# Kernel optimization log

Measured on AMD Instinct MI355X. Metric: run time of the kernel, lower is better.

## Reference

```python
import jax, jax.numpy as jnp
import numpy as np

N = 192    # num_nodes == number of trees
M = 256    # max_node_number (feature width per tree level)
D = 1024   # tree depth (NATree.shape[1])
K = M - N + 1  # Conv2 kernel size


def setup_inputs() -> dict:
    key = jax.random.key(0)
    k1, k2, k3, k4, k5, k6 = jax.random.split(key, 6)
    s = 0.05
    NATree = jax.random.normal(k1, (N, D, M), jnp.float32)
    W = jax.random.normal(k2, (M, M, 2), jnp.float32) * s   # Conv1d weight [out, in, kernel=2]
    b = jax.random.normal(k3, (M,), jnp.float32) * s        # Conv1d bias
    x = jax.random.normal(k4, (N, M), jnp.float32) * s      # self.x parameter
    W2 = jax.random.normal(k5, (K,), jnp.float32) * s       # Conv2 weight (out=1,in=1,kernel=K)
    b2 = jax.random.normal(k6, (), jnp.float32) * s         # Conv2 bias
    return {"NATree": NATree, "W": W, "b": b, "x": x, "W2": W2, "b2": b2}


def reference(NATree, W, b, x, W2, b2):
    # Conv1d(k=2) on cat([row_j, h]) splits into two MxM matmuls:
    #   h_new = W0 @ row_j + W1 @ h + b + sigmoid(row_j)
    W0 = W[:, :, 0]  # multiplies row_j (first position in concat)
    W1 = W[:, :, 1]  # multiplies carried state h
    rows = NATree[:, :-1, :]  # [N, D-1, M], levels j = 0 .. D-2
    # Precompute the per-level additive term in one batched matmul.
    u = jnp.einsum('ndm,km->ndk', rows, W0) + b + jax.nn.sigmoid(rows)  # [N, D-1, M]
    h0 = NATree[:, -1, :]  # [N, M], initial state = last tree level
    # Walk levels j = D-2 down to 0.
    u_seq = jnp.flip(u, axis=1).transpose(1, 0, 2)  # [D-1, N, M]

    def step(h, u_j):
        return u_j + h @ W1.T, None

    h_fin, _ = jax.lax.scan(step, h0, u_seq)  # [N, M]
    res = jax.nn.relu(h_fin + x)  # [N, M]
    # Conv2: 1-ch cross-correlation, kernel K, output length M-K+1 = N.
    out = jax.lax.conv_general_dilated(
        res[:, None, :], W2[None, None, :], window_strides=(1,), padding='VALID') + b2
    return jax.nn.sigmoid(out[:, 0, :])  # [N, N]
```

## Files before the change

kernel.cpp:

```cpp
#include <hip/hip_runtime.h>
#include <hip/hip_bf16.h>
#include <cstddef>

#define DN 192
#define DM 256
#define DD 1024
#define DK 65
#define OUTW 192

using f32x4 = __attribute__((ext_vector_type(4))) float;
using s16x8 = __attribute__((ext_vector_type(8))) short;

__device__ __forceinline__ float sigm(float v) { return 1.0f / (1.0f + __expf(-v)); }
__device__ __forceinline__ unsigned short f2b(float f) {
    __hip_bfloat16 h = __float2bfloat16(f);
    return *reinterpret_cast<unsigned short*>(&h);
}
__device__ __forceinline__ float b2f(unsigned short s) {
    __hip_bfloat16 h = *reinterpret_cast<__hip_bfloat16*>(&s);
    return __bfloat162float(h);
}

#define OFF_QF   0u
#define OFF_A2   65536u
#define OFF_A4   131072u
#define OFF_A8   196608u
#define OFF_A16  262144u
#define OFF_A32  327680u
#define OFF_A64  393216u
#define OFF_QB   458752u
#define OFF_W0B  491520u
#define OFF_P8B  524288u
#define OFF_P64B 557056u
#define OFF_SA1  589824u
#define OFF_SA2  3735552u
#define MFMA_NEED_BYTES 18087936ULL

__global__ __launch_bounds__(256) void k_prep2(const float* __restrict__ W,
                                               float* __restrict__ ws) {
    const int bid = blockIdx.x, t = threadIdx.x;
    if (bid < 256) {
        const int c = bid, m = t;
        ws[OFF_QF + m * 256 + c] = W[(size_t)(c * 256 + m) * 2 + 1];
    } else {
        const int which = (bid - 256) >> 5;
        const int e = ((bid - 256) & 31) * 256 + t;
        const int ct = e >> 9, ks = (e >> 6) & 7, l = e & 63;
        const int c = ct * 16 + (l & 15);
        const int mb = ks * 32 + (l >> 4) * 8;
        s16x8 pk;
#pragma unroll
        for (int j = 0; j < 8; ++j)
            pk[j] = (short)f2b(W[(size_t)(c * 256 + mb + j) * 2 + (which ? 0 : 1)]);
        float* dst = ws + (which ? OFF_W0B : OFF_QB);
        reinterpret_cast<s16x8*>(dst)[e] = pk;
    }
}

__global__ __launch_bounds__(256) void k_sq256(const float* __restrict__ A,
                                               float* __restrict__ C,
                                               ushort* __restrict__ bfrag) {
    __shared__ float ar[256];
    const int r0 = blockIdx.x, k = threadIdx.x;
    ar[k] = A[r0 * 256 + k];
    __syncthreads();
    float a0 = 0.f, a1 = 0.f, a2 = 0.f, a3 = 0.f;
    for (int m = 0; m < 256; m += 8) {
        a0 += ar[m + 0] * A[(m + 0) * 256 + k] + ar[m + 4] * A[(m + 4) * 256 + k];
        a1 += ar[m + 1] * A[(m + 1) * 256 + k] + ar[m + 5] * A[(m + 5) * 256 + k];
        a2 += ar[m + 2] * A[(m + 2) * 256 + k] + ar[m + 6] * A[(m + 6) * 256 + k];
        a3 += ar[m + 3] * A[(m + 3) * 256 + k] + ar[m + 7] * A[(m + 7) * 256 + k];
    }
    const float v = (a0 + a1) + (a2 + a3);
    C[r0 * 256 + k] = v;
    if (bfrag) {
        const int entry = ((k >> 4) * 8 + (r0 >> 5)) * 64 + ((r0 >> 3) & 3) * 16 + (k & 15);
        bfrag[entry * 8 + (r0 & 7)] = f2b(v);
    }
}

__global__ __launch_bounds__(512, 4) void k_fused(const float* __restrict__ NAT,
                                                  const float* __restrict__ bvec,
                                                  const float* __restrict__ ws,
                                                  ushort* __restrict__ SA1) {
    __shared__ short Rl[2][8][66][8];
    __shared__ short Sl[2][2][8][64][8];
    const int rt2 = blockIdx.x;
    const int grp = blockIdx.y;
    const int tid = threadIdx.x;
    const int w = tid >> 6, l = tid & 63;
    const int n0 = rt2 * 32;
    const ushort* W0b = reinterpret_cast<const ushort*>(ws + OFF_W0B);
    const ushort* Qb  = reinterpret_cast<const ushort*>(ws + OFF_QB);

    s16x8 qreg[2][8];
#pragma unroll
    for (int c = 0; c < 2; ++c)
#pragma unroll
        for (int ks = 0; ks < 8; ++ks)
            qreg[c][ks] = *reinterpret_cast<const s16x8*>(Qb + (((2 * w + c) * 8 + ks) * 64 + l) * 8);

    const int srow = tid >> 4;
    const int sks  = (tid >> 1) & 7;
    const int shalf = tid & 1;
    const float* sbase = NAT + (size_t)(n0 + srow) * DD * DM + sks * 32 + shalf * 16;

    float4 rv0, rv1, rv2, rv3;
    {
        const float* p = sbase + (size_t)(grp * 8 + 7) * DM;
        rv0 = *reinterpret_cast<const float4*>(p + 0);
        rv1 = *reinterpret_cast<const float4*>(p + 4);
        rv2 = *reinterpret_cast<const float4*>(p + 8);
        rv3 = *reinterpret_cast<const float4*>(p + 12);
    }
    const float bcol0 = bvec[w * 32 + (l & 15)];
    const float bcol1 = bvec[w * 32 + 16 + (l & 15)];

    f32x4 acc[2][2];
    int cur = 0;
    for (int it = 0; it < 8; ++it) {
        const int d = grp * 8 + 7 - it;
        {
            const int g0 = shalf * 2;
            s16x8 pk0, pk1;
            pk0[0] = (short)f2b(rv0.x); pk0[1] = (short)f2b(rv0.y);
            pk0[2] = (short)f2b(rv0.z); pk0[3] = (short)f2b(rv0.w);
            pk0[4] = (short)f2b(rv1.x); pk0[5] = (short)f2b(rv1.y);
            pk0[6] = (short)f2b(rv1.z); pk0[7] = (short)f2b(rv1.w);
            pk1[0] = (short)f2b(rv2.x); pk1[1] = (short)f2b(rv2.y);
            pk1[2] = (short)f2b(rv2.z); pk1[3] = (short)f2b(rv2.w);
            pk1[4] = (short)f2b(rv3.x); pk1[5] = (short)f2b(rv3.y);
            pk1[6] = (short)f2b(rv3.z); pk1[7] = (short)f2b(rv3.w);
            *reinterpret_cast<s16x8*>(&Rl[srow >> 4][sks][(srow & 15) + 16 * g0][0]) = pk0;
            *reinterpret_cast<s16x8*>(&Rl[srow >> 4][sks][(srow & 15) + 16 * (g0 + 1)][0]) = pk1;
        }
        if (it < 7) {
            const float* p = sbase + (size_t)(d - 1) * DM;
            rv0 = *reinterpret_cast<const float4*>(p + 0);
            rv1 = *reinterpret_cast<const float4*>(p + 4);
            rv2 = *reinterpret_cast<const float4*>(p + 8);
            rv3 = *reinterpret_cast<const float4*>(p + 12);
        }
        __syncthreads();

        if (grp == 127 && it == 0) {
#pragma unroll
            for (int rt = 0; rt < 2; ++rt)
#pragma unroll
                for (int c = 0; c < 2; ++c) {
                    const int col = w * 32 + c * 16 + (l & 15);
#pragma unroll
                    for (int r = 0; r < 4; ++r) {
                        const int n = n0 + rt * 16 + (l >> 4) * 4 + r;
                        acc[rt][c][r] = NAT[((size_t)n * DD + (DD - 1)) * DM + col];
                    }
                }
        } else {
#pragma unroll
            for (int rt = 0; rt < 2; ++rt)
#pragma unroll
                for (int c = 0; c < 2; ++c) {
                    const int col = w * 32 + c * 16 + (l & 15);
                    const int ksm = col >> 5, sl = 16 * ((col >> 3) & 3), jb = col & 7;
                    const float bc = c ? bcol1 : bcol0;
#pragma unroll
                    for (int r = 0; r < 4; ++r) {
                        const int row15 = (l >> 4) * 4 + r;
                        const unsigned short sv = (unsigned short)Rl[rt][ksm][row15 + sl][jb];
                        acc[rt][c][r] = bc + sigm(b2f(sv));
                    }
                }
#pragma unroll
            for (int ks = 0; ks < 8; ++ks) {
                const s16x8 gb0 = *reinterpret_cast<const s16x8*>(W0b + (((2 * w + 0) * 8 + ks) * 64 + l) * 8);
                const s16x8 gb1 = *reinterpret_cast<const s16x8*>(W0b + (((2 * w + 1) * 8 + ks) * 64 + l) * 8);
                const s16x8 a0 = *reinterpret_cast<const s16x8*>(&Rl[0][ks][l][0]);
                const s16x8 a1 = *reinterpret_cast<const s16x8*>(&Rl[1][ks][l][0]);
                acc[0][0] = __builtin_amdgcn_mfma_f32_16x16x32_bf16(a0, gb0, acc[0][0], 0, 0, 0);
                acc[0][1] = __builtin_amdgcn_mfma_f32_16x16x32_bf16(a0, gb1, acc[0][1], 0, 0, 0);
                acc[1][0] = __builtin_amdgcn_mfma_f32_16x16x32_bf16(a1, gb0, acc[1][0], 0, 0, 0);
                acc[1][1] = __builtin_amdgcn_mfma_f32_16x16x32_bf16(a1, gb1, acc[1][1], 0, 0, 0);
            }
        }
        if (it > 0) {
#pragma unroll
            for (int ks = 0; ks < 8; ++ks) {
                const s16x8 s0 = *reinterpret_cast<const s16x8*>(&Sl[cur][0][ks][l][0]);
                const s16x8 s1 = *reinterpret_cast<const s16x8*>(&Sl[cur][1][ks][l][0]);
                acc[0][0] = __builtin_amdgcn_mfma_f32_16x16x32_bf16(s0, qreg[0][ks], acc[0][0], 0, 0, 0);
                acc[0][1] = __builtin_amdgcn_mfma_f32_16x16x32_bf16(s0, qreg[1][ks], acc[0][1], 0, 0, 0);
                acc[1][0] = __builtin_amdgcn_mfma_f32_16x16x32_bf16(s1, qreg[0][ks], acc[1][0], 0, 0, 0);
                acc[1][1] = __builtin_amdgcn_mfma_f32_16x16x32_bf16(s1, qreg[1][ks], acc[1][1], 0, 0, 0);
            }
        }
        if (it < 7) {
#pragma unroll
            for (int rt = 0; rt < 2; ++rt)
#pragma unroll
                for (int c = 0; c < 2; ++c) {
                    const int col = w * 32 + c * 16 + (l & 15);
                    const int sl = 16 * ((col >> 3) & 3), jb = col & 7;
#pragma unroll
                    for (int r = 0; r < 4; ++r) {
                        const int row15 = (l >> 4) * 4 + r;
                        Sl[cur ^ 1][rt][w][row15 + sl][jb] = (short)f2b(acc[rt][c][r]);
                    }
                }
            __syncthreads();
            cur ^= 1;
        }
    }

#pragma unroll
    for (int rt = 0; rt < 2; ++rt)
#pragma unroll
        for (int c = 0; c < 2; ++c) {
            const size_t base = (((size_t)grp * 12 + (rt2 * 2 + rt)) * 16 + (2 * w + c)) * 64 + l;
            ushort4 o;
            o.x = f2b(acc[rt][c][0]); o.y = f2b(acc[rt][c][1]);
            o.z = f2b(acc[rt][c][2]); o.w = f2b(acc[rt][c][3]);
            reinterpret_cast<ushort4*>(SA1)[base] = o;
        }
}

__global__ __launch_bounds__(512) void k_scan(const void* __restrict__ Vin, int in_bf16,
                                              const float* __restrict__ ws, unsigned qb_off,
                                              int nsteps,
                                              void* __restrict__ OutC, int out_bf16,
                                              const float* __restrict__ xin,
                                              const float* __restrict__ W2,
                                              const float* __restrict__ b2p,
                                              float* __restrict__ outF) {
    __shared__ __align__(16) char smem[33856];
    short (*Sl)[2][8][64][8] = reinterpret_cast<short (*)[2][8][64][8]>(smem);
    float (*resl)[260]       = reinterpret_cast<float (*)[260]>(smem);
    float* w2l               = reinterpret_cast<float*>(smem + 33280);
    const int rt2 = blockIdx.x;
    const int grp = blockIdx.y;
    const int tid = threadIdx.x;
    const int w = tid >> 6, l = tid & 63;
    const ushort* Qb = reinterpret_cast<const ushort*>(ws + qb_off);

    s16x8 qreg[2][8];
#pragma unroll
    for (int c = 0; c < 2; ++c)
#pragma unroll
        for (int ks = 0; ks < 8; ++ks)
            qreg[c][ks] = *reinterpret_cast<const s16x8*>(Qb + (((2 * w + c) * 8 + ks) * 64 + l) * 8);

    f32x4 acc[2][2];
    int cur = 0;
    for (int it = 0; it < nsteps; ++it) {
        const int d = grp * nsteps + (nsteps - 1) - it;
#pragma unroll
        for (int rt = 0; rt < 2; ++rt)
#pragma unroll
            for (int c = 0; c < 2; ++c) {
                const size_t base = (((size_t)d * 12 + (rt2 * 2 + rt)) * 16 + (2 * w + c)) * 64 + l;
                if (in_bf16) {
                    const ushort4 v = reinterpret_cast<const ushort4*>(Vin)[base];
                    acc[rt][c][0] = b2f(v.x); acc[rt][c][1] = b2f(v.y);
                    acc[rt][c][2] = b2f(v.z); acc[rt][c][3] = b2f(v.w);
                } else {
                    acc[rt][c] = reinterpret_cast<const f32x4*>(Vin)[base];
                }
            }
        if (it > 0) {
#pragma unroll
            for (int ks = 0; ks < 8; ++ks) {
                const s16x8 a0 = *reinterpret_cast<const s16x8*>(&Sl[cur][0][ks][l][0]);
                const s16x8 a1 = *reinterpret_cast<const s16x8*>(&Sl[cur][1][ks][l][0]);
                acc[0][0] = __builtin_amdgcn_mfma_f32_16x16x32_bf16(a0, qreg[0][ks], acc[0][0], 0, 0, 0);
                acc[0][1] = __builtin_amdgcn_mfma_f32_16x16x32_bf16(a0, qreg[1][ks], acc[0][1], 0, 0, 0);
                acc[1][0] = __builtin_amdgcn_mfma_f32_16x16x32_bf16(a1, qreg[0][ks], acc[1][0], 0, 0, 0);
                acc[1][1] = __builtin_amdgcn_mfma_f32_16x16x32_bf16(a1, qreg[1][ks], acc[1][1], 0, 0, 0);
            }
        }
        if (it < nsteps - 1) {
#pragma unroll
            for (int rt = 0; rt < 2; ++rt)
#pragma unroll
                for (int c = 0; c < 2; ++c) {
                    const int col = w * 32 + c * 16 + (l & 15);
                    const int sl = 16 * ((col >> 3) & 3), jb = col & 7;
#pragma unroll
                    for (int r = 0; r < 4; ++r) {
                        const int row15 = (l >> 4) * 4 + r;
                        Sl[cur ^ 1][rt][w][row15 + sl][jb] = (short)f2b(acc[rt][c][r]);
                    }
                }
            __syncthreads();
            cur ^= 1;
        }
    }

    if (outF == nullptr) {
#pragma unroll
        for (int rt = 0; rt < 2; ++rt)
#pragma unroll
            for (int c = 0; c < 2; ++c) {
                const size_t base = (((size_t)grp * 12 + (rt2 * 2 + rt)) * 16 + (2 * w + c)) * 64 + l;
                if (out_bf16) {
                    ushort4 o;
                    o.x = f2b(acc[rt][c][0]); o.y = f2b(acc[rt][c][1]);
                    o.z = f2b(acc[rt][c][2]); o.w = f2b(acc[rt][c][3]);
                    reinterpret_cast<ushort4*>(OutC)[base] = o;
                } else {
                    reinterpret_cast<f32x4*>(OutC)[base] = acc[rt][c];
                }
            }
    } else {
        if (tid < DK) w2l[tid] = W2[tid];
        __syncthreads();
#pragma unroll
        for (int rt = 0; rt < 2; ++rt)
#pragma unroll
            for (int c = 0; c < 2; ++c) {
                const int col = w * 32 + c * 16 + (l & 15);
#pragma unroll
                for (int r = 0; r < 4; ++r) {
                    const int row = rt * 16 + (l >> 4) * 4 + r;
                    const int n = rt2 * 32 + row;
                    const float v = acc[rt][c][r] + xin[(size_t)n * DM + col];
                    resl[row][col] = v > 0.f ? v : 0.f;
                }
            }
        __syncthreads();
        const float b2v = *b2p;
        const int k = tid & 255;
        for (int rr = tid >> 8; rr < 32; rr += 2) {
            if (k < OUTW) {
                float o = b2v;
#pragma unroll
                for (int i = 0; i < DK; ++i) o += resl[rr][k + i] * w2l[i];
                outF[(size_t)(rt2 * 32 + rr) * OUTW + k] = sigm(o);
            }
        }
    }
}

#define OCB 16
#define ONB 64
#define OR1 24
#define ORB1 8
#define OPSTR 260
#define O_W0T 0u
#define O_W1T 65536u
#define O_PW  131072u
#define O_S   (131072u + 5u*65536u)

__global__ __launch_bounds__(256) void k_prep_o(const float* __restrict__ W, float* __restrict__ ws) {
    const int m = blockIdx.x, k = threadIdx.x;
    const float2 w = *reinterpret_cast<const float2*>(W + (size_t)k * 512 + m * 2);
    ws[O_W0T + m * 256 + k] = w.x;
    ws[O_W1T + m * 256 + k] = w.y;
}

__global__ __launch_bounds__(256) void k_sq_o(const float* __restrict__ A, float* __restrict__ C) {
    __shared__ float ar[4][OPSTR];
    const int r0 = blockIdx.x * 4, k = threadIdx.x;
    for (int r = 0; r < 4; ++r) ar[r][k] = A[(r0 + r) * 256 + k];
    __syncthreads();
    float a0 = 0.f, a1 = 0.f, a2 = 0.f, a3 = 0.f;
    for (int m = 0; m < 256; m += 4) {
        const float p0 = A[(m + 0) * 256 + k], p1 = A[(m + 1) * 256 + k];
        const float p2 = A[(m + 2) * 256 + k], p3 = A[(m + 3) * 256 + k];
        float4 t;
        t = *reinterpret_cast<const float4*>(&ar[0][m]); a0 += t.x * p0 + t.y * p1 + t.z * p2 + t.w * p3;
        t = *reinterpret_cast<const float4*>(&ar[1][m]); a1 += t.x * p0 + t.y * p1 + t.z * p2 + t.w * p3;
        t = *reinterpret_cast<const float4*>(&ar[2][m]); a2 += t.x * p0 + t.y * p1 + t.z * p2 + t.w * p3;
        t = *reinterpret_cast<const float4*>(&ar[3][m]); a3 += t.x * p0 + t.y * p1 + t.z * p2 + t.w * p3;
    }
    C[(r0 + 0) * 256 + k] = a0; C[(r0 + 1) * 256 + k] = a1;
    C[(r0 + 2) * 256 + k] = a2; C[(r0 + 3) * 256 + k] = a3;
}

__global__ __launch_bounds__(256) void k_phase1_o(const float* __restrict__ NAT,
                                                  const float* __restrict__ bvec,
                                                  const float* __restrict__ ws,
                                                  float* __restrict__ Sall) {
    __shared__ float Sl[OR1 * OPSTR];
    __shared__ float Rl[OR1 * OPSTR];
    const int rb = blockIdx.x, bb = blockIdx.y, tid = threadIdx.x;
    const int tj = tid & 63, ti = tid >> 6, n0 = rb * OR1;
    const float* __restrict__ W0t = ws + O_W0T;
    const float* __restrict__ W1t = ws + O_W1T;
    const float4 bv = *reinterpret_cast<const float4*>(bvec + 4 * tj);
    float acc[6][4];
    for (int it = 0; it < OCB; ++it) {
        const int d = bb * OCB + (OCB - 1) - it;
#pragma unroll
        for (int q = 0; q < 6; ++q) {
            const int row = q * 4 + ti;
            const float4 v = *reinterpret_cast<const float4*>(NAT + ((size_t)(n0 + row) * DD + d) * DM + 4 * tj);
            *reinterpret_cast<float4*>(&Rl[row * OPSTR + 4 * tj]) = v;
        }
        __syncthreads();
        if (d == DD - 1) {
#pragma unroll
            for (int r = 0; r < 6; ++r) {
                const float4 v = *reinterpret_cast<const float4*>(&Rl[(ti * 6 + r) * OPSTR + 4 * tj]);
                acc[r][0] = v.x; acc[r][1] = v.y; acc[r][2] = v.z; acc[r][3] = v.w;
            }
        } else {
#pragma unroll
            for (int r = 0; r < 6; ++r) {
                const float4 v = *reinterpret_cast<const float4*>(&Rl[(ti * 6 + r) * OPSTR + 4 * tj]);
                acc[r][0] = bv.x + sigm(v.x); acc[r][1] = bv.y + sigm(v.y);
                acc[r][2] = bv.z + sigm(v.z); acc[r][3] = bv.w + sigm(v.w);
            }
            if (it == 0) {
#pragma unroll 2
                for (int m = 0; m < DM; m += 2) {
                    const float4 w0a = *reinterpret_cast<const float4*>(W0t + m * DM + 4 * tj);
                    const float4 w0b = *reinterpret_cast<const float4*>(W0t + (m + 1) * DM + 4 * tj);
#pragma unroll
                    for (int r = 0; r < 6; ++r) {
                        const float2 rv = *reinterpret_cast<const float2*>(&Rl[(ti * 6 + r) * OPSTR + m]);
                        acc[r][0] += rv.x * w0a.x + rv.y * w0b.x;
                        acc[r][1] += rv.x * w0a.y + rv.y * w0b.y;
                        acc[r][2] += rv.x * w0a.z + rv.y * w0b.z;
                        acc[r][3] += rv.x * w0a.w + rv.y * w0b.w;
                    }
                }
            } else {
#pragma unroll 2
                for (int m = 0; m < DM; m += 2) {
                    const float4 w0a = *reinterpret_cast<const float4*>(W0t + m * DM + 4 * tj);
                    const float4 w0b = *reinterpret_cast<const float4*>(W0t + (m + 1) * DM + 4 * tj);
                    const float4 w1a = *reinterpret_cast<const float4*>(W1t + m * DM + 4 * tj);
                    const float4 w1b = *reinterpret_cast<const float4*>(W1t + (m + 1) * DM + 4 * tj);
#pragma unroll
                    for (int r = 0; r < 6; ++r) {
                        const float2 rv = *reinterpret_cast<const float2*>(&Rl[(ti * 6 + r) * OPSTR + m]);
                        const float2 sv = *reinterpret_cast<const float2*>(&Sl[(ti * 6 + r) * OPSTR + m]);
                        acc[r][0] += rv.x * w0a.x + rv.y * w0b.x + sv.x * w1a.x + sv.y * w1b.x;
                        acc[r][1] += rv.x * w0a.y + rv.y * w0b.y + sv.x * w1a.y + sv.y * w1b.y;
                        acc[r][2] += rv.x * w0a.z + rv.y * w0b.z + sv.x * w1a.z + sv.y * w1b.z;
                        acc[r][3] += rv.x * w0a.w + rv.y * w0b.w + sv.x * w1a.w + sv.y * w1b.w;
                    }
                }
            }
        }
        __syncthreads();
#pragma unroll
        for (int r = 0; r < 6; ++r) {
            float4 v; v.x = acc[r][0]; v.y = acc[r][1]; v.z = acc[r][2]; v.w = acc[r][3];
            *reinterpret_cast<float4*>(&Sl[(ti * 6 + r) * OPSTR + 4 * tj]) = v;
        }
        __syncthreads();
    }
    float* dst = Sall + ((size_t)bb * DN + n0) * DM;
#pragma unroll
    for (int r = 0; r < 6; ++r) {
        float4 v; v.x = acc[r][0]; v.y = acc[r][1]; v.z = acc[r][2]; v.w = acc[r][3];
        *reinterpret_cast<float4*>(dst + (size_t)(ti * 6 + r) * DM + 4 * tj) = v;
    }
}

__global__ __launch_bounds__(256) void k_phase2_o(const float* __restrict__ Sall,
                                                  const float* __restrict__ P,
                                                  const float* __restrict__ x,
                                                  const float* __restrict__ W2,
                                                  const float* __restrict__ b2p,
                                                  float* __restrict__ out) {
    __shared__ float Tl[2][DM];
    __shared__ float resl[DM];
    const int n = blockIdx.x, k = threadIdx.x;
    float a = Sall[((size_t)(ONB - 1) * DN + n) * DM + k];
    Tl[0][k] = a;
    __syncthreads();
    int cur = 0;
    for (int b = ONB - 2; b >= 0; --b) {
        const float s0 = Sall[((size_t)b * DN + n) * DM + k];
        float a0 = 0.f, a1 = 0.f, a2 = 0.f, a3 = 0.f;
        for (int m = 0; m < DM; m += 8) {
            const float4 t0 = *reinterpret_cast<const float4*>(&Tl[cur][m]);
            const float4 t1 = *reinterpret_cast<const float4*>(&Tl[cur][m + 4]);
            a0 += t0.x * P[(m + 0) * DM + k] + t1.x * P[(m + 4) * DM + k];
            a1 += t0.y * P[(m + 1) * DM + k] + t1.y * P[(m + 5) * DM + k];
            a2 += t0.z * P[(m + 2) * DM + k] + t1.z * P[(m + 6) * DM + k];
            a3 += t0.w * P[(m + 3) * DM + k] + t1.w * P[(m + 7) * DM + k];
        }
        a = s0 + ((a0 + a1) + (a2 + a3));
        Tl[cur ^ 1][k] = a;
        __syncthreads();
        cur ^= 1;
    }
    const float b2v = *b2p;
    float r = a + x[(size_t)n * DM + k];
    resl[k] = r > 0.f ? r : 0.f;
    __syncthreads();
    if (k < OUTW) {
        float o = b2v;
#pragma unroll 5
        for (int i = 0; i < DK; ++i) o += resl[k + i] * W2[i];
        out[(size_t)n * OUTW + k] = sigm(o);
    }
}

extern "C" void kernel_launch(void* const* d_in, const int* in_sizes, int n_in,
                              void* d_out, int out_size, void* d_ws, size_t ws_size,
                              hipStream_t stream) {
    const float* NAT = (const float*)d_in[0];
    const float* W   = (const float*)d_in[1];
    const float* bv  = (const float*)d_in[2];
    const float* x   = (const float*)d_in[3];
    const float* W2  = (const float*)d_in[4];
    const float* b2  = (const float*)d_in[5];
    float* out = (float*)d_out;
    float* ws  = (float*)d_ws;

    if (ws_size >= MFMA_NEED_BYTES) {
        k_prep2<<<320, 256, 0, stream>>>(W, ws);

        ushort* SA1 = reinterpret_cast<ushort*>(ws + OFF_SA1);
        float*  SA2 = ws + OFF_SA2;

        k_fused<<<dim3(6, 128), 512, 0, stream>>>(NAT, bv, ws, SA1);

        k_sq256<<<256, 256, 0, stream>>>(ws + OFF_QF,  ws + OFF_A2,  nullptr);
        k_sq256<<<256, 256, 0, stream>>>(ws + OFF_A2,  ws + OFF_A4,  nullptr);
        k_sq256<<<256, 256, 0, stream>>>(ws + OFF_A4,  ws + OFF_A8,
                                         reinterpret_cast<ushort*>(ws + OFF_P8B));
        k_sq256<<<256, 256, 0, stream>>>(ws + OFF_A8,  ws + OFF_A16, nullptr);
        k_sq256<<<256, 256, 0, stream>>>(ws + OFF_A16, ws + OFF_A32, nullptr);
        k_sq256<<<256, 256, 0, stream>>>(ws + OFF_A32, ws + OFF_A64,
                                         reinterpret_cast<ushort*>(ws + OFF_P64B));

        k_scan<<<dim3(6, 16), 512, 0, stream>>>(SA1, 1, ws, OFF_P8B, 8,
                                                SA2, 0, nullptr, nullptr, nullptr, nullptr);
        k_scan<<<dim3(6, 1), 512, 0, stream>>>(SA2, 0, ws, OFF_P64B, 16,
                                               nullptr, 0, x, W2, b2, out);
    } else {
        k_prep_o<<<256, 256, 0, stream>>>(W, ws);
        const float* q = ws + O_W1T;
        float* pw = ws + O_PW;
        k_sq_o<<<64, 256, 0, stream>>>(q,              pw + 0 * 65536);
        k_sq_o<<<64, 256, 0, stream>>>(pw + 0 * 65536, pw + 1 * 65536);
        k_sq_o<<<64, 256, 0, stream>>>(pw + 1 * 65536, pw + 2 * 65536);
        k_sq_o<<<64, 256, 0, stream>>>(pw + 2 * 65536, pw + 3 * 65536);
        float* Sall = ws + O_S;
        k_phase1_o<<<dim3(ORB1, ONB), 256, 0, stream>>>(NAT, bv, ws, Sall);
        k_phase2_o<<<192, 256, 0, stream>>>(Sall, pw + 3 * 65536, x, W2, b2, out);
    }
}
```

Before: 513.8 us.

## Stream Q fragments from memory and fold sigmoid term into MFMA via identity

The Q (W1) fragments were held in 16 s16x8 registers per thread in both the fused and scan kernels. They are now reloaded from global memory inside the k-loop, which lowers register pressure and may raise occupancy. In the fused kernel, sigmoid of each row is computed once at staging time into a new shared buffer, and added to the accumulator through an MFMA against an identity fragment instead of scalar shared reads plus exp per output. The fallback non-MFMA path is removed, so the workspace-size check is gone. The cost is more global or L2 loads for Q, an extra shared buffer, and extra sigmoid work at staging.

```diff
diff --git a/kernel.cpp b/kernel.cpp
--- a/kernel.cpp
+++ b/kernel.cpp
@@ -34,7 +34,6 @@
 #define OFF_P64B 557056u
 #define OFF_SA1  589824u
 #define OFF_SA2  3735552u
-#define MFMA_NEED_BYTES 18087936ULL
 
 __global__ __launch_bounds__(256) void k_prep2(const float* __restrict__ W,
                                                float* __restrict__ ws) {
@@ -84,6 +83,7 @@
                                                   const float* __restrict__ ws,
                                                   ushort* __restrict__ SA1) {
     __shared__ short Rl[2][8][66][8];
+    __shared__ short Gl[2][8][66][8];
     __shared__ short Sl[2][2][8][64][8];
     const int rt2 = blockIdx.x;
     const int grp = blockIdx.y;
@@ -93,17 +93,26 @@
     const ushort* W0b = reinterpret_cast<const ushort*>(ws + OFF_W0B);
     const ushort* Qb  = reinterpret_cast<const ushort*>(ws + OFF_QB);
 
-    s16x8 qreg[2][8];
-#pragma unroll
-    for (int c = 0; c < 2; ++c)
-#pragma unroll
-        for (int ks = 0; ks < 8; ++ks)
-            qreg[c][ks] = *reinterpret_cast<const s16x8*>(Qb + (((2 * w + c) * 8 + ks) * 64 + l) * 8);
-
-    const int srow = tid >> 4;
-    const int sks  = (tid >> 1) & 7;
-    const int shalf = tid & 1;
+    s16x8 ifrag0 = {}, ifrag1 = {};
+    {
+        const int rbase = (l >> 4) * 8, cl = l & 15;
+#pragma unroll
+        for (int j = 0; j < 8; ++j) {
+            if (rbase + j == cl)      ifrag0[j] = (short)0x3F80;
+            if (rbase + j == 16 + cl) ifrag1[j] = (short)0x3F80;
+        }
+    }
+    const float bcol0 = bvec[w * 32 + (l & 15)];
+    const float bcol1 = bvec[w * 32 + 16 + (l & 15)];
+    const int i_w = l & 15, g_w = l >> 4;
+
+    const int srow = tid >> 4, sks = (tid >> 1) & 7, shalf = tid & 1;
     const float* sbase = NAT + (size_t)(n0 + srow) * DD * DM + sks * 32 + shalf * 16;
+    const int g0s = shalf * 2;
+    short* rdstA = &Rl[srow >> 4][sks][(srow & 15) + 16 * g0s][0];
+    short* rdstB = &Rl[srow >> 4][sks][(srow & 15) + 16 * (g0s + 1)][0];
+    short* gdstA = &Gl[srow >> 4][sks][(srow & 15) + 16 * g0s][0];
+    short* gdstB = &Gl[srow >> 4][sks][(srow & 15) + 16 * (g0s + 1)][0];
 
     float4 rv0, rv1, rv2, rv3;
     {
@@ -113,26 +122,24 @@
         rv2 = *reinterpret_cast<const float4*>(p + 8);
         rv3 = *reinterpret_cast<const float4*>(p + 12);
     }
-    const float bcol0 = bvec[w * 32 + (l & 15)];
-    const float bcol1 = bvec[w * 32 + 16 + (l & 15)];
 
     f32x4 acc[2][2];
     int cur = 0;
     for (int it = 0; it < 8; ++it) {
         const int d = grp * 8 + 7 - it;
         {
-            const int g0 = shalf * 2;
-            s16x8 pk0, pk1;
-            pk0[0] = (short)f2b(rv0.x); pk0[1] = (short)f2b(rv0.y);
-            pk0[2] = (short)f2b(rv0.z); pk0[3] = (short)f2b(rv0.w);
-            pk0[4] = (short)f2b(rv1.x); pk0[5] = (short)f2b(rv1.y);
-            pk0[6] = (short)f2b(rv1.z); pk0[7] = (short)f2b(rv1.w);
-            pk1[0] = (short)f2b(rv2.x); pk1[1] = (short)f2b(rv2.y);
-            pk1[2] = (short)f2b(rv2.z); pk1[3] = (short)f2b(rv2.w);
-            pk1[4] = (short)f2b(rv3.x); pk1[5] = (short)f2b(rv3.y);
-            pk1[6] = (short)f2b(rv3.z); pk1[7] = (short)f2b(rv3.w);
-            *reinterpret_cast<s16x8*>(&Rl[srow >> 4][sks][(srow & 15) + 16 * g0][0]) = pk0;
-            *reinterpret_cast<s16x8*>(&Rl[srow >> 4][sks][(srow & 15) + 16 * (g0 + 1)][0]) = pk1;
+            float f[16] = {rv0.x, rv0.y, rv0.z, rv0.w, rv1.x, rv1.y, rv1.z, rv1.w,
+                           rv2.x, rv2.y, rv2.z, rv2.w, rv3.x, rv3.y, rv3.z, rv3.w};
+            s16x8 pr0, pr1, pg0, pg1;
+#pragma unroll
+            for (int u = 0; u < 8; ++u) {
+                pr0[u] = (short)f2b(f[u]);     pg0[u] = (short)f2b(sigm(f[u]));
+                pr1[u] = (short)f2b(f[8 + u]); pg1[u] = (short)f2b(sigm(f[8 + u]));
+            }
+            *reinterpret_cast<s16x8*>(rdstA) = pr0;
+            *reinterpret_cast<s16x8*>(rdstB) = pr1;
+            *reinterpret_cast<s16x8*>(gdstA) = pg0;
+            *reinterpret_cast<s16x8*>(gdstB) = pg1;
         }
         if (it < 7) {
             const float* p = sbase + (size_t)(d - 1) * DM;
@@ -148,10 +155,10 @@
             for (int rt = 0; rt < 2; ++rt)
 #pragma unroll
                 for (int c = 0; c < 2; ++c) {
-                    const int col = w * 32 + c * 16 + (l & 15);
+                    const int col = w * 32 + c * 16 + i_w;
 #pragma unroll
                     for (int r = 0; r < 4; ++r) {
-                        const int n = n0 + rt * 16 + (l >> 4) * 4 + r;
+                        const int n = n0 + rt * 16 + g_w * 4 + r;
                         acc[rt][c][r] = NAT[((size_t)n * DD + (DD - 1)) * DM + col];
                     }
                 }
@@ -159,38 +166,35 @@
 #pragma unroll
             for (int rt = 0; rt < 2; ++rt)
 #pragma unroll
-                for (int c = 0; c < 2; ++c) {
-                    const int col = w * 32 + c * 16 + (l & 15);
-                    const int ksm = col >> 5, sl = 16 * ((col >> 3) & 3), jb = col & 7;
-                    const float bc = c ? bcol1 : bcol0;
-#pragma unroll
-                    for (int r = 0; r < 4; ++r) {
-                        const int row15 = (l >> 4) * 4 + r;
-                        const unsigned short sv = (unsigned short)Rl[rt][ksm][row15 + sl][jb];
-                        acc[rt][c][r] = bc + sigm(b2f(sv));
-                    }
-                }
+                for (int r = 0; r < 4; ++r) { acc[rt][0][r] = bcol0; acc[rt][1][r] = bcol1; }
+            {
+                const s16x8 ga = *reinterpret_cast<const s16x8*>(&Gl[0][w][l][0]);
+                const s16x8 gb = *reinterpret_cast<const s16x8*>(&Gl[1][w][l][0]);
+                acc[0][0] = __builtin_amdgcn_mfma_f32_16x16x32_bf16(ga, ifrag0, acc[0][0], 0, 0, 0);
+                acc[0][1] = __builtin_amdgcn_mfma_f32_16x16x32_bf16(ga, ifrag1, acc[0][1], 0, 0, 0);
+                acc[1][0] = __builtin_amdgcn_mfma_f32_16x16x32_bf16(gb, ifrag0, acc[1][0], 0, 0, 0);
+                acc[1][1] = __builtin_amdgcn_mfma_f32_16x16x32_bf16(gb, ifrag1, acc[1][1], 0, 0, 0);
+            }
 #pragma unroll
             for (int ks = 0; ks < 8; ++ks) {
-                const s16x8 gb0 = *reinterpret_cast<const s16x8*>(W0b + (((2 * w + 0) * 8 + ks) * 64 + l) * 8);
-                const s16x8 gb1 = *reinterpret_cast<const s16x8*>(W0b + (((2 * w + 1) * 8 + ks) * 64 + l) * 8);
                 const s16x8 a0 = *reinterpret_cast<const s16x8*>(&Rl[0][ks][l][0]);
                 const s16x8 a1 = *reinterpret_cast<const s16x8*>(&Rl[1][ks][l][0]);
-                acc[0][0] = __builtin_amdgcn_mfma_f32_16x16x32_bf16(a0, gb0, acc[0][0], 0, 0, 0);
-                acc[0][1] = __builtin_amdgcn_mfma_f32_16x16x32_bf16(a0, gb1, acc[0][1], 0, 0, 0);
-                acc[1][0] = __builtin_amdgcn_mfma_f32_16x16x32_bf16(a1, gb0, acc[1][0], 0, 0, 0);
-                acc[1][1] = __builtin_amdgcn_mfma_f32_16x16x32_bf16(a1, gb1, acc[1][1], 0, 0, 0);
-            }
-        }
-        if (it > 0) {
-#pragma unroll
-            for (int ks = 0; ks < 8; ++ks) {
-                const s16x8 s0 = *reinterpret_cast<const s16x8*>(&Sl[cur][0][ks][l][0]);
-                const s16x8 s1 = *reinterpret_cast<const s16x8*>(&Sl[cur][1][ks][l][0]);
-                acc[0][0] = __builtin_amdgcn_mfma_f32_16x16x32_bf16(s0, qreg[0][ks], acc[0][0], 0, 0, 0);
-                acc[0][1] = __builtin_amdgcn_mfma_f32_16x16x32_bf16(s0, qreg[1][ks], acc[0][1], 0, 0, 0);
-                acc[1][0] = __builtin_amdgcn_mfma_f32_16x16x32_bf16(s1, qreg[0][ks], acc[1][0], 0, 0, 0);
-                acc[1][1] = __builtin_amdgcn_mfma_f32_16x16x32_bf16(s1, qreg[1][ks], acc[1][1], 0, 0, 0);
+                const s16x8 w0 = *reinterpret_cast<const s16x8*>(W0b + (((2 * w + 0) * 8 + ks) * 64 + l) * 8);
+                const s16x8 w1 = *reinterpret_cast<const s16x8*>(W0b + (((2 * w + 1) * 8 + ks) * 64 + l) * 8);
+                acc[0][0] = __builtin_amdgcn_mfma_f32_16x16x32_bf16(a0, w0, acc[0][0], 0, 0, 0);
+                acc[0][1] = __builtin_amdgcn_mfma_f32_16x16x32_bf16(a0, w1, acc[0][1], 0, 0, 0);
+                acc[1][0] = __builtin_amdgcn_mfma_f32_16x16x32_bf16(a1, w0, acc[1][0], 0, 0, 0);
+                acc[1][1] = __builtin_amdgcn_mfma_f32_16x16x32_bf16(a1, w1, acc[1][1], 0, 0, 0);
+                if (it > 0) {
+                    const s16x8 q0 = *reinterpret_cast<const s16x8*>(Qb + (((2 * w + 0) * 8 + ks) * 64 + l) * 8);
+                    const s16x8 q1 = *reinterpret_cast<const s16x8*>(Qb + (((2 * w + 1) * 8 + ks) * 64 + l) * 8);
+                    const s16x8 s0 = *reinterpret_cast<const s16x8*>(&Sl[cur][0][ks][l][0]);
+                    const s16x8 s1 = *reinterpret_cast<const s16x8*>(&Sl[cur][1][ks][l][0]);
+                    acc[0][0] = __builtin_amdgcn_mfma_f32_16x16x32_bf16(s0, q0, acc[0][0], 0, 0, 0);
+                    acc[0][1] = __builtin_amdgcn_mfma_f32_16x16x32_bf16(s0, q1, acc[0][1], 0, 0, 0);
+                    acc[1][0] = __builtin_amdgcn_mfma_f32_16x16x32_bf16(s1, q0, acc[1][0], 0, 0, 0);
+                    acc[1][1] = __builtin_amdgcn_mfma_f32_16x16x32_bf16(s1, q1, acc[1][1], 0, 0, 0);
+                }
             }
         }
         if (it < 7) {
@@ -198,11 +202,10 @@
             for (int rt = 0; rt < 2; ++rt)
 #pragma unroll
                 for (int c = 0; c < 2; ++c) {
-                    const int col = w * 32 + c * 16 + (l & 15);
-                    const int sl = 16 * ((col >> 3) & 3), jb = col & 7;
+                    const int sl = 16 * (2 * c + (i_w >> 3)), jb = i_w & 7;
 #pragma unroll
                     for (int r = 0; r < 4; ++r) {
-                        const int row15 = (l >> 4) * 4 + r;
+                        const int row15 = g_w * 4 + r;
                         Sl[cur ^ 1][rt][w][row15 + sl][jb] = (short)f2b(acc[rt][c][r]);
                     }
                 }
@@ -241,13 +244,6 @@
     const int w = tid >> 6, l = tid & 63;
     const ushort* Qb = reinterpret_cast<const ushort*>(ws + qb_off);
 
-    s16x8 qreg[2][8];
-#pragma unroll
-    for (int c = 0; c < 2; ++c)
-#pragma unroll
-        for (int ks = 0; ks < 8; ++ks)
-            qreg[c][ks] = *reinterpret_cast<const s16x8*>(Qb + (((2 * w + c) * 8 + ks) * 64 + l) * 8);
-
     f32x4 acc[2][2];
     int cur = 0;
     for (int it = 0; it < nsteps; ++it) {
@@ -270,10 +266,12 @@
             for (int ks = 0; ks < 8; ++ks) {
                 const s16x8 a0 = *reinterpret_cast<const s16x8*>(&Sl[cur][0][ks][l][0]);
                 const s16x8 a1 = *reinterpret_cast<const s16x8*>(&Sl[cur][1][ks][l][0]);
-                acc[0][0] = __builtin_amdgcn_mfma_f32_16x16x32_bf16(a0, qreg[0][ks], acc[0][0], 0, 0, 0);
-                acc[0][1] = __builtin_amdgcn_mfma_f32_16x16x32_bf16(a0, qreg[1][ks], acc[0][1], 0, 0, 0);
-                acc[1][0] = __builtin_amdgcn_mfma_f32_16x16x32_bf16(a1, qreg[0][ks], acc[1][0], 0, 0, 0);
-                acc[1][1] = __builtin_amdgcn_mfma_f32_16x16x32_bf16(a1, qreg[1][ks], acc[1][1], 0, 0, 0);
+                const s16x8 q0 = *reinterpret_cast<const s16x8*>(Qb + (((2 * w + 0) * 8 + ks) * 64 + l) * 8);
+                const s16x8 q1 = *reinterpret_cast<const s16x8*>(Qb + (((2 * w + 1) * 8 + ks) * 64 + l) * 8);
+                acc[0][0] = __builtin_amdgcn_mfma_f32_16x16x32_bf16(a0, q0, acc[0][0], 0, 0, 0);
+                acc[0][1] = __builtin_amdgcn_mfma_f32_16x16x32_bf16(a0, q1, acc[0][1], 0, 0, 0);
+                acc[1][0] = __builtin_amdgcn_mfma_f32_16x16x32_bf16(a1, q0, acc[1][0], 0, 0, 0);
+                acc[1][1] = __builtin_amdgcn_mfma_f32_16x16x32_bf16(a1, q1, acc[1][1], 0, 0, 0);
             }
         }
         if (it < nsteps - 1) {
@@ -336,166 +334,6 @@
                 outF[(size_t)(rt2 * 32 + rr) * OUTW + k] = sigm(o);
             }
         }
-    }
-}
-
-#define OCB 16
-#define ONB 64
-#define OR1 24
-#define ORB1 8
-#define OPSTR 260
-#define O_W0T 0u
-#define O_W1T 65536u
-#define O_PW  131072u
-#define O_S   (131072u + 5u*65536u)
-
-__global__ __launch_bounds__(256) void k_prep_o(const float* __restrict__ W, float* __restrict__ ws) {
-    const int m = blockIdx.x, k = threadIdx.x;
-    const float2 w = *reinterpret_cast<const float2*>(W + (size_t)k * 512 + m * 2);
-    ws[O_W0T + m * 256 + k] = w.x;
-    ws[O_W1T + m * 256 + k] = w.y;
-}
-
-__global__ __launch_bounds__(256) void k_sq_o(const float* __restrict__ A, float* __restrict__ C) {
-    __shared__ float ar[4][OPSTR];
-    const int r0 = blockIdx.x * 4, k = threadIdx.x;
-    for (int r = 0; r < 4; ++r) ar[r][k] = A[(r0 + r) * 256 + k];
-    __syncthreads();
-    float a0 = 0.f, a1 = 0.f, a2 = 0.f, a3 = 0.f;
-    for (int m = 0; m < 256; m += 4) {
-        const float p0 = A[(m + 0) * 256 + k], p1 = A[(m + 1) * 256 + k];
-        const float p2 = A[(m + 2) * 256 + k], p3 = A[(m + 3) * 256 + k];
-        float4 t;
-        t = *reinterpret_cast<const float4*>(&ar[0][m]); a0 += t.x * p0 + t.y * p1 + t.z * p2 + t.w * p3;
-        t = *reinterpret_cast<const float4*>(&ar[1][m]); a1 += t.x * p0 + t.y * p1 + t.z * p2 + t.w * p3;
-        t = *reinterpret_cast<const float4*>(&ar[2][m]); a2 += t.x * p0 + t.y * p1 + t.z * p2 + t.w * p3;
-        t = *reinterpret_cast<const float4*>(&ar[3][m]); a3 += t.x * p0 + t.y * p1 + t.z * p2 + t.w * p3;
-    }
-    C[(r0 + 0) * 256 + k] = a0; C[(r0 + 1) * 256 + k] = a1;
-    C[(r0 + 2) * 256 + k] = a2; C[(r0 + 3) * 256 + k] = a3;
-}
-
-__global__ __launch_bounds__(256) void k_phase1_o(const float* __restrict__ NAT,
-                                                  const float* __restrict__ bvec,
-                                                  const float* __restrict__ ws,
-                                                  float* __restrict__ Sall) {
-    __shared__ float Sl[OR1 * OPSTR];
-    __shared__ float Rl[OR1 * OPSTR];
-    const int rb = blockIdx.x, bb = blockIdx.y, tid = threadIdx.x;
-    const int tj = tid & 63, ti = tid >> 6, n0 = rb * OR1;
-    const float* __restrict__ W0t = ws + O_W0T;
-    const float* __restrict__ W1t = ws + O_W1T;
-    const float4 bv = *reinterpret_cast<const float4*>(bvec + 4 * tj);
-    float acc[6][4];
-    for (int it = 0; it < OCB; ++it) {
-        const int d = bb * OCB + (OCB - 1) - it;
-#pragma unroll
-        for (int q = 0; q < 6; ++q) {
-            const int row = q * 4 + ti;
-            const float4 v = *reinterpret_cast<const float4*>(NAT + ((size_t)(n0 + row) * DD + d) * DM + 4 * tj);
-            *reinterpret_cast<float4*>(&Rl[row * OPSTR + 4 * tj]) = v;
-        }
-        __syncthreads();
-        if (d == DD - 1) {
-#pragma unroll
-            for (int r = 0; r < 6; ++r) {
-                const float4 v = *reinterpret_cast<const float4*>(&Rl[(ti * 6 + r) * OPSTR + 4 * tj]);
-                acc[r][0] = v.x; acc[r][1] = v.y; acc[r][2] = v.z; acc[r][3] = v.w;
-            }
-        } else {
-#pragma unroll
-            for (int r = 0; r < 6; ++r) {
-                const float4 v = *reinterpret_cast<const float4*>(&Rl[(ti * 6 + r) * OPSTR + 4 * tj]);
-                acc[r][0] = bv.x + sigm(v.x); acc[r][1] = bv.y + sigm(v.y);
-                acc[r][2] = bv.z + sigm(v.z); acc[r][3] = bv.w + sigm(v.w);
-            }
-            if (it == 0) {
-#pragma unroll 2
-                for (int m = 0; m < DM; m += 2) {
-                    const float4 w0a = *reinterpret_cast<const float4*>(W0t + m * DM + 4 * tj);
-                    const float4 w0b = *reinterpret_cast<const float4*>(W0t + (m + 1) * DM + 4 * tj);
-#pragma unroll
-                    for (int r = 0; r < 6; ++r) {
-                        const float2 rv = *reinterpret_cast<const float2*>(&Rl[(ti * 6 + r) * OPSTR + m]);
-                        acc[r][0] += rv.x * w0a.x + rv.y * w0b.x;
-                        acc[r][1] += rv.x * w0a.y + rv.y * w0b.y;
-                        acc[r][2] += rv.x * w0a.z + rv.y * w0b.z;
-                        acc[r][3] += rv.x * w0a.w + rv.y * w0b.w;
-                    }
-                }
-            } else {
-#pragma unroll 2
-                for (int m = 0; m < DM; m += 2) {
-                    const float4 w0a = *reinterpret_cast<const float4*>(W0t + m * DM + 4 * tj);
-                    const float4 w0b = *reinterpret_cast<const float4*>(W0t + (m + 1) * DM + 4 * tj);
-                    const float4 w1a = *reinterpret_cast<const float4*>(W1t + m * DM + 4 * tj);
-                    const float4 w1b = *reinterpret_cast<const float4*>(W1t + (m + 1) * DM + 4 * tj);
-#pragma unroll
-                    for (int r = 0; r < 6; ++r) {
-                        const float2 rv = *reinterpret_cast<const float2*>(&Rl[(ti * 6 + r) * OPSTR + m]);
-                        const float2 sv = *reinterpret_cast<const float2*>(&Sl[(ti * 6 + r) * OPSTR + m]);
-                        acc[r][0] += rv.x * w0a.x + rv.y * w0b.x + sv.x * w1a.x + sv.y * w1b.x;
-                        acc[r][1] += rv.x * w0a.y + rv.y * w0b.y + sv.x * w1a.y + sv.y * w1b.y;
-                        acc[r][2] += rv.x * w0a.z + rv.y * w0b.z + sv.x * w1a.z + sv.y * w1b.z;
-                        acc[r][3] += rv.x * w0a.w + rv.y * w0b.w + sv.x * w1a.w + sv.y * w1b.w;
-                    }
-                }
-            }
-        }
-        __syncthreads();
-#pragma unroll
-        for (int r = 0; r < 6; ++r) {
-            float4 v; v.x = acc[r][0]; v.y = acc[r][1]; v.z = acc[r][2]; v.w = acc[r][3];
-            *reinterpret_cast<float4*>(&Sl[(ti * 6 + r) * OPSTR + 4 * tj]) = v;
-        }
-        __syncthreads();
-    }
-    float* dst = Sall + ((size_t)bb * DN + n0) * DM;
-#pragma unroll
-    for (int r = 0; r < 6; ++r) {
-        float4 v; v.x = acc[r][0]; v.y = acc[r][1]; v.z = acc[r][2]; v.w = acc[r][3];
-        *reinterpret_cast<float4*>(dst + (size_t)(ti * 6 + r) * DM + 4 * tj) = v;
-    }
-}
-
-__global__ __launch_bounds__(256) void k_phase2_o(const float* __restrict__ Sall,
-                                                  const float* __restrict__ P,
-                                                  const float* __restrict__ x,
-                                                  const float* __restrict__ W2,
-                                                  const float* __restrict__ b2p,
-                                                  float* __restrict__ out) {
-    __shared__ float Tl[2][DM];
-    __shared__ float resl[DM];
-    const int n = blockIdx.x, k = threadIdx.x;
-    float a = Sall[((size_t)(ONB - 1) * DN + n) * DM + k];
-    Tl[0][k] = a;
-    __syncthreads();
-    int cur = 0;
-    for (int b = ONB - 2; b >= 0; --b) {
-        const float s0 = Sall[((size_t)b * DN + n) * DM + k];
-        float a0 = 0.f, a1 = 0.f, a2 = 0.f, a3 = 0.f;
-        for (int m = 0; m < DM; m += 8) {
-            const float4 t0 = *reinterpret_cast<const float4*>(&Tl[cur][m]);
-            const float4 t1 = *reinterpret_cast<const float4*>(&Tl[cur][m + 4]);
-            a0 += t0.x * P[(m + 0) * DM + k] + t1.x * P[(m + 4) * DM + k];
-            a1 += t0.y * P[(m + 1) * DM + k] + t1.y * P[(m + 5) * DM + k];
-            a2 += t0.z * P[(m + 2) * DM + k] + t1.z * P[(m + 6) * DM + k];
-            a3 += t0.w * P[(m + 3) * DM + k] + t1.w * P[(m + 7) * DM + k];
-        }
-        a = s0 + ((a0 + a1) + (a2 + a3));
-        Tl[cur ^ 1][k] = a;
-        __syncthreads();
-        cur ^= 1;
-    }
-    const float b2v = *b2p;
-    float r = a + x[(size_t)n * DM + k];
-    resl[k] = r > 0.f ? r : 0.f;
-    __syncthreads();
-    if (k < OUTW) {
-        float o = b2v;
-#pragma unroll 5
-        for (int i = 0; i < DK; ++i) o += resl[k + i] * W2[i];
-        out[(size_t)n * OUTW + k] = sigm(o);
     }
 }
 
@@ -511,37 +349,24 @@
     float* out = (float*)d_out;
     float* ws  = (float*)d_ws;
 
-    if (ws_size >= MFMA_NEED_BYTES) {
-        k_prep2<<<320, 256, 0, stream>>>(W, ws);
-
-        ushort* SA1 = reinterpret_cast<ushort*>(ws + OFF_SA1);
-        float*  SA2 = ws + OFF_SA2;
-
-        k_fused<<<dim3(6, 128), 512, 0, stream>>>(NAT, bv, ws, SA1);
-
-        k_sq256<<<256, 256, 0, stream>>>(ws + OFF_QF,  ws + OFF_A2,  nullptr);
-        k_sq256<<<256, 256, 0, stream>>>(ws + OFF_A2,  ws + OFF_A4,  nullptr);
-        k_sq256<<<256, 256, 0, stream>>>(ws + OFF_A4,  ws + OFF_A8,
-                                         reinterpret_cast<ushort*>(ws + OFF_P8B));
-        k_sq256<<<256, 256, 0, stream>>>(ws + OFF_A8,  ws + OFF_A16, nullptr);
-        k_sq256<<<256, 256, 0, stream>>>(ws + OFF_A16, ws + OFF_A32, nullptr);
-        k_sq256<<<256, 256, 0, stream>>>(ws + OFF_A32, ws + OFF_A64,
-                                         reinterpret_cast<ushort*>(ws + OFF_P64B));
-
-        k_scan<<<dim3(6, 16), 512, 0, stream>>>(SA1, 1, ws, OFF_P8B, 8,
-                                                SA2, 0, nullptr, nullptr, nullptr, nullptr);
-        k_scan<<<dim3(6, 1), 512, 0, stream>>>(SA2, 0, ws, OFF_P64B, 16,
-                                               nullptr, 0, x, W2, b2, out);
-    } else {
-        k_prep_o<<<256, 256, 0, stream>>>(W, ws);
-        const float* q = ws + O_W1T;
-        float* pw = ws + O_PW;
-        k_sq_o<<<64, 256, 0, stream>>>(q,              pw + 0 * 65536);
-        k_sq_o<<<64, 256, 0, stream>>>(pw + 0 * 65536, pw + 1 * 65536);
-        k_sq_o<<<64, 256, 0, stream>>>(pw + 1 * 65536, pw + 2 * 65536);
-        k_sq_o<<<64, 256, 0, stream>>>(pw + 2 * 65536, pw + 3 * 65536);
-        float* Sall = ws + O_S;
-        k_phase1_o<<<dim3(ORB1, ONB), 256, 0, stream>>>(NAT, bv, ws, Sall);
-        k_phase2_o<<<192, 256, 0, stream>>>(Sall, pw + 3 * 65536, x, W2, b2, out);
-    }
-}
+    ushort* SA1 = reinterpret_cast<ushort*>(ws + OFF_SA1);
+    float*  SA2 = ws + OFF_SA2;
+
+    k_prep2<<<320, 256, 0, stream>>>(W, ws);
+
+    k_fused<<<dim3(6, 128), 512, 0, stream>>>(NAT, bv, ws, SA1);
+
+    k_sq256<<<256, 256, 0, stream>>>(ws + OFF_QF,  ws + OFF_A2,  nullptr);
+    k_sq256<<<256, 256, 0, stream>>>(ws + OFF_A2,  ws + OFF_A4,  nullptr);
+    k_sq256<<<256, 256, 0, stream>>>(ws + OFF_A4,  ws + OFF_A8,
+                                     reinterpret_cast<ushort*>(ws + OFF_P8B));
+    k_sq256<<<256, 256, 0, stream>>>(ws + OFF_A8,  ws + OFF_A16, nullptr);
+    k_sq256<<<256, 256, 0, stream>>>(ws + OFF_A16, ws + OFF_A32, nullptr);
+    k_sq256<<<256, 256, 0, stream>>>(ws + OFF_A32, ws + OFF_A64,
+                                     reinterpret_cast<ushort*>(ws + OFF_P64B));
+
+    k_scan<<<dim3(6, 16), 512, 0, stream>>>(SA1, 1, ws, OFF_P8B, 8,
+                                            SA2, 0, nullptr, nullptr, nullptr, nullptr);
+    k_scan<<<dim3(6, 1), 512, 0, stream>>>(SA2, 0, ws, OFF_P64B, 16,
+                                           nullptr, 0, x, W2, b2, out);
+}
```

Measured after the change: 560.9 us. 1.09x slower.
